# Optimization experiments

Measured on AMD Instinct MI355X. Metric: run time of the kernel, lower is better.

## Reference

```python
import jax, jax.numpy as jnp
import numpy as np

BATCH, IN_SIZE, CH, DIM, MODES, LAYERS, PROJ, OUT = 16, 1, 128, 128, 32, 4, 128, 1


def setup_inputs() -> dict:
    key = jax.random.key(0)
    ks = jax.random.split(key, 12)
    scale = 1.0 / (CH * CH)
    inp = {
        "z": jax.random.normal(ks[0], (BATCH, IN_SIZE, DIM, DIM), dtype=jnp.float32),
        # Lifting: pointwise linear input_size -> channels
        "lift_w": jax.random.normal(ks[1], (CH, IN_SIZE), dtype=jnp.float32) / np.sqrt(IN_SIZE),
        "lift_b": jnp.zeros((CH,), dtype=jnp.float32),
        # Spectral conv weights per layer, two mode corners, complex stored as real/imag
        "wr1": scale * jax.random.normal(ks[2], (LAYERS, CH, CH, MODES, MODES), dtype=jnp.float32),
        "wi1": scale * jax.random.normal(ks[3], (LAYERS, CH, CH, MODES, MODES), dtype=jnp.float32),
        "wr2": scale * jax.random.normal(ks[4], (LAYERS, CH, CH, MODES, MODES), dtype=jnp.float32),
        "wi2": scale * jax.random.normal(ks[5], (LAYERS, CH, CH, MODES, MODES), dtype=jnp.float32),
        # Projection: channels -> projection_size -> output_size (pointwise MLP)
        "pw1": jax.random.normal(ks[6], (PROJ, CH), dtype=jnp.float32) / np.sqrt(CH),
        "pb1": jnp.zeros((PROJ,), dtype=jnp.float32),
        "pw2": jax.random.normal(ks[7], (OUT, PROJ), dtype=jnp.float32) / np.sqrt(PROJ),
        "pb2": jnp.zeros((OUT,), dtype=jnp.float32),
    }
    return inp


def _spectral_conv(v, w1, w2, modes, size):
    # v: [b, c, X, Y] real; rfft2 over last two dims (norm='backward')
    vf = jnp.fft.rfft2(v, norm="backward")  # [b, c, X, Y//2+1] complex
    of = jnp.zeros_like(vf)
    # low-frequency corner
    of = of.at[:, :, :modes, :modes].set(
        jnp.einsum("bixy,ioxy->boxy", vf[:, :, :modes, :modes], w1))
    # high (negative) frequency corner along first spatial axis
    of = of.at[:, :, -modes:, :modes].set(
        jnp.einsum("bixy,ioxy->boxy", vf[:, :, -modes:, :modes], w2))
    return jnp.fft.irfft2(of, s=(size, size), norm="backward")


def reference(z, lift_w, lift_b, wr1, wi1, wr2, wi2, pw1, pb1, pw2, pb2):
    n_layers = wr1.shape[0]
    modes = wr1.shape[-1]
    size = z.shape[-1]
    # Lifting: [b, in, x, y] -> [b, ch, x, y]
    v = jnp.einsum("bixy,ci->bcxy", z, lift_w) + lift_b[None, :, None, None]
    out = v
    for l in range(n_layers):
        w1 = wr1[l] + 1j * wi1[l]
        w2 = wr2[l] + 1j * wi2[l]
        out = _spectral_conv(out, w1, w2, modes, size)
    # Projection MLP (pointwise over grid)
    h = jnp.einsum("bcxy,pc->bpxy", out, pw1) + pb1[None, :, None, None]
    h = jax.nn.gelu(h)
    out = jnp.einsum("bpxy,op->boxy", h, pw2) + pb2[None, :, None, None]
    return out
```

## Files before the change

kernel.cpp:

```cpp
#include <hip/hip_runtime.h>
#include <math.h>

#define B 16
#define CH 128
#define DIM 128
#define MODES 32
#define NLAYERS 4
#define PROJ 128
#define U 64
#define KY 32
#define NMODE (U*KY)
#define N2 (DIM*DIM)
#define PG 32
#define PPG (PROJ/PG)

__device__ __forceinline__ void async16(const void* g, void* l) {
  __builtin_amdgcn_global_load_lds((const __attribute__((address_space(1))) unsigned int*)g,
                                   (__attribute__((address_space(3))) unsigned int*)l, 16, 0, 0);
}

__global__ __launch_bounds__(256) void k_zf1(const float* __restrict__ z,
                                             float2* __restrict__ t1) {
  __shared__ float zrow[16][DIM];
  __shared__ float2 tw[DIM];
  int bid = blockIdx.x;
  int b = bid >> 3, xt = bid & 7;
  int x0 = xt * 16;
  int t = threadIdx.x;
  if (t < 128) {
    float ang = (float)(2.0 * M_PI) * (float)t / 128.0f;
    tw[t] = make_float2(cosf(ang), sinf(ang));
  }
  for (int e = t; e < 16 * DIM / 4; e += 256)
    ((float4*)&zrow[0][0])[e] = ((const float4*)&z[b * N2 + x0 * DIM])[e];
  __syncthreads();
  #pragma unroll
  for (int j = 0; j < 2; ++j) {
    int it = t + j * 256;
    int x_l = it >> 5, ky = it & 31;
    float tr = 0.f, ti = 0.f;
    for (int y = 0; y < DIM; ++y) {
      float v = zrow[x_l][y];
      float2 w = tw[(ky * y) & 127];
      tr += v * w.x;
      ti -= v * w.y;
    }
    t1[((size_t)b * DIM + x0 + x_l) * KY + ky] = make_float2(tr, ti);
  }
}

__global__ __launch_bounds__(256) void k_zf2(const float2* __restrict__ t1,
                                             float* __restrict__ zfr, float* __restrict__ zfi) {
  __shared__ float2 t1s[DIM][KY];
  __shared__ float2 tw[DIM];
  int bid = blockIdx.x;
  int b = bid >> 1, uh = bid & 1;
  int t = threadIdx.x;
  if (t < 128) {
    float ang = (float)(2.0 * M_PI) * (float)t / 128.0f;
    tw[t] = make_float2(cosf(ang), sinf(ang));
  }
  for (int e = t; e < DIM * KY / 2; e += 256)
    ((float4*)&t1s[0][0])[e] = ((const float4*)&t1[(size_t)b * DIM * KY])[e];
  __syncthreads();
  #pragma unroll
  for (int j = 0; j < 4; ++j) {
    int m = t + j * 256;
    int u_l = m >> 5, ky = m & 31;
    int u = uh * 32 + u_l;
    int kx = (u < 32) ? u : (u + 64);
    float ar = 0.f, ai = 0.f;
    for (int x = 0; x < DIM; ++x) {
      float2 v = t1s[x][ky];
      float2 w = tw[(kx * x) & 127];
      ar += v.x * w.x + v.y * w.y;
      ai += v.y * w.x - v.x * w.y;
    }
    zfr[b * NMODE + u * KY + ky] = ar;
    zfi[b * NMODE + u * KY + ky] = ai;
  }
}

__global__ __launch_bounds__(256) void k_lift(const float* __restrict__ zfr, const float* __restrict__ zfi,
                                              const float* __restrict__ lw, const float* __restrict__ lb,
                                              float2* __restrict__ vcout) {
  int idx = blockIdx.x * 256 + threadIdx.x;
  if (idx >= B * CH * NMODE) return;
  int m = idx & (NMODE - 1);
  int c = (idx >> 11) & 127;
  int b = idx >> 18;
  float w = lw[c];
  float re = w * zfr[b * NMODE + m];
  float im = w * zfi[b * NMODE + m];
  if (m == 0) re += 16384.f * lb[c];
  vcout[idx] = make_float2(re, im);
}

__global__ __launch_bounds__(256) void k_spec(const float2* __restrict__ vc,
                                              const float* __restrict__ wr1, const float* __restrict__ wi1,
                                              const float* __restrict__ wr2, const float* __restrict__ wi2,
                                              float2* __restrict__ oc) {
  __shared__ float lW[2][2][2][8][32];
  __shared__ float2 lV[2][2][16][32];
  int bid = blockIdx.x;
  int u = ((bid & 7) << 3) | ((bid >> 3) & 7);
  int ot = bid >> 6;
  int o0 = ot * 8;
  int kxw = u & 31;
  const float* wr = (u >= 32) ? wr2 : wr1;
  const float* wi = (u >= 32) ? wi2 : wi1;
  int t = threadIdx.x;
  int ky = t & 31, bh = (t >> 5) & 1, oq = t >> 6;
  int wv = t >> 6, lane = t & 63;
  float accR[2][8] = {}, accI[2][8] = {};

  #define STAGE(bf, i0)                                                              \
    {                                                                                \
      _Pragma("unroll")                                                              \
      for (int n = 0; n < 3; ++n) {                                                  \
        int nu = wv * 3 + n;                                                         \
        if (nu < 4) {                                                                \
          int ri = nu >> 1, il = nu & 1;                                             \
          int o_l = lane >> 3, ky4 = (lane & 7) * 4;                                 \
          const float* src = (ri ? wi : wr) +                                        \
            (((size_t)((i0) + il) * CH + o0 + o_l) * MODES + kxw) * MODES + ky4;     \
          async16(src, (char*)&lW[bf][0][0][0][0] + (size_t)nu * 1024 + lane * 16);  \
        } else {                                                                     \
          int nv = nu - 4;                                                           \
          int il = nv >> 2;                                                          \
          int b_l = (nv & 3) * 4 + (lane >> 4), ky2 = (lane & 15) * 2;               \
          const float2* src = vc + ((size_t)b_l * CH + (i0) + il) * NMODE +          \
                              u * KY + ky2;                                          \
          async16(src, (char*)&lV[bf][0][0][0] + (size_t)nv * 1024 + lane * 16);     \
        }                                                                            \
      }                                                                              \
    }

  STAGE(0, 0);
  for (int k = 0; k < 64; ++k) {
    int cur = k & 1;
    __syncthreads();
    if (k + 1 < 64) STAGE(cur ^ 1, (k + 1) * 2);
    #pragma unroll
    for (int il = 0; il < 2; ++il) {
      float wrv[2], wiv[2];
      #pragma unroll
      for (int j = 0; j < 2; ++j) {
        wrv[j] = lW[cur][0][il][oq * 2 + j][ky];
        wiv[j] = lW[cur][1][il][oq * 2 + j][ky];
      }
      #pragma unroll
      for (int bb = 0; bb < 8; ++bb) {
        float2 v = lV[cur][il][bh * 8 + bb][ky];
        #pragma unroll
        for (int j = 0; j < 2; ++j) {
          accR[j][bb] += wrv[j] * v.x - wiv[j] * v.y;
          accI[j][bb] += wrv[j] * v.y + wiv[j] * v.x;
        }
      }
    }
  }
  #undef STAGE
  #pragma unroll
  for (int j = 0; j < 2; ++j)
    #pragma unroll
    for (int bb = 0; bb < 8; ++bb) {
      int o = o0 + oq * 2 + j, b = bh * 8 + bb;
      oc[(((size_t)b * CH + o) * U + u) * KY + ky] = make_float2(accR[j][bb], accI[j][bb]);
    }
}

__global__ __launch_bounds__(256) void k_proj0(float2* __restrict__ vc) {
  int idx = blockIdx.x * 256 + threadIdx.x;
  if (idx >= B * CH * 33) return;
  int pi = idx % 33;
  int bc = idx / 33;
  float2* base = vc + (size_t)bc * NMODE;
  if (pi == 0) {
    base[0].y = 0.f;
  } else if (pi == 32) {
    base[32 * KY].x *= 0.5f;
    base[32 * KY].y *= 0.5f;
  } else {
    int ua = pi, ub = 64 - pi;
    float2 a = base[ua * KY], b2 = base[ub * KY];
    base[ua * KY] = make_float2(0.5f * (a.x + b2.x), 0.5f * (a.y - b2.y));
    base[ub * KY] = make_float2(0.5f * (b2.x + a.x), 0.5f * (b2.y - a.y));
  }
}

__global__ __launch_bounds__(256) void k_pw1(const float2* __restrict__ xc,
                                             const float* __restrict__ pw1,
                                             float2* __restrict__ hc) {
  __shared__ float wT[CH][CH + 1];
  int bid = blockIdx.x;
  int b = ((bid & 7) << 1) | ((bid >> 8) & 1);
  int jt = (bid >> 3) & 31;
  int t = threadIdx.x;
  for (int e = t; e < CH * CH; e += 256) {
    int p = e >> 7, c = e & 127;
    wT[c][p] = pw1[e];
  }
  __syncthreads();
  int tx = t & 15, ty = t >> 4;
  int j0 = jt * 64 + tx * 4;
  float accR[4][8] = {}, accI[4][8] = {};
  for (int c = 0; c < CH; ++c) {
    const float4* x4 = (const float4*)&xc[((size_t)b * CH + c) * NMODE + j0];
    float4 v0 = x4[0], v1 = x4[1];
    float xrv[4] = {v0.x, v0.z, v1.x, v1.z};
    float xiv[4] = {v0.y, v0.w, v1.y, v1.w};
    float w[8];
    #pragma unroll
    for (int pp = 0; pp < 8; ++pp) w[pp] = wT[c][ty * 8 + pp];
    #pragma unroll
    for (int jj = 0; jj < 4; ++jj)
      #pragma unroll
      for (int pp = 0; pp < 8; ++pp) {
        accR[jj][pp] += w[pp] * xrv[jj];
        accI[jj][pp] += w[pp] * xiv[jj];
      }
  }
  #pragma unroll
  for (int pp = 0; pp < 8; ++pp) {
    int p = ty * 8 + pp;
    float4* o4 = (float4*)&hc[((size_t)b * CH + p) * NMODE + j0];
    o4[0] = make_float4(accR[0][pp], accI[0][pp], accR[1][pp], accI[1][pp]);
    o4[1] = make_float4(accR[2][pp], accI[2][pp], accR[3][pp], accI[3][pp]);
  }
}

__global__ __launch_bounds__(256) void k_idft_partial(const float2* __restrict__ hc,
                                                      const float* __restrict__ pb1,
                                                      const float* __restrict__ pw2,
                                                      float* __restrict__ partial) {
  __shared__ float2 tw[DIM];
  __shared__ float2 hfs[2][NMODE];
  __shared__ float2 sbuf[16][KY];
  int bid = blockIdx.x;
  int b = (bid & 7) | (((bid >> 3) & 1) << 3);
  int pg = (bid >> 4) & 31, xs = bid >> 9;
  int x0 = xs * 8;
  int t = threadIdx.x;
  int wv = t >> 6, lane = t & 63;
  if (t < 128) {
    float ang = (float)(2.0 * M_PI) * (float)t / 128.0f;
    tw[t] = make_float2(cosf(ang), sinf(ang));
  }

  #define STAGE_H(bf, pp_)                                                           \
    {                                                                                \
      const char* srcb = (const char*)(hc + ((size_t)b * CH + pg * PPG + (pp_)) * NMODE); \
      _Pragma("unroll")                                                              \
      for (int n = 0; n < 4; ++n) {                                                  \
        int nu = wv * 4 + n;                                                         \
        async16(srcb + (size_t)nu * 1024 + lane * 16,                                \
                (char*)&hfs[bf][0] + (size_t)nu * 1024 + lane * 16);                 \
      }                                                                              \
    }

  STAGE_H(0, 0);
  __syncthreads();
  int y = t & 63, xh = t >> 6;
  float Cr[KY], Sr[KY];
  #pragma unroll
  for (int ky = 0; ky < KY; ++ky) {
    float2 w = tw[(ky * y) & 127];
    float wk = (ky == 0) ? 1.f : 2.f;
    Cr[ky] = wk * w.x;
    Sr[ky] = -wk * w.y;
  }
  int xqA = t >> 5, kyA = t & 31;
  int xA = x0 + xqA;
  float res[8] = {0.f, 0.f, 0.f, 0.f, 0.f, 0.f, 0.f, 0.f};
  for (int pp = 0; pp < PPG; ++pp) {
    int p = pg * PPG + pp;
    int cur = pp & 1;
    if (pp) __syncthreads();
    if (pp + 1 < PPG) STAGE_H(cur ^ 1, pp + 1);
    {
      float per = 0.f, pei = 0.f, por = 0.f, poi = 0.f;
      #pragma unroll
      for (int uu = 0; uu < 32; uu += 2) {
        float2 w0 = tw[(uu * xA) & 127];
        float2 h0 = hfs[cur][uu * KY + kyA];
        per += h0.x * w0.x - h0.y * w0.y;
        pei += h0.x * w0.y + h0.y * w0.x;
        float2 w1 = tw[((uu + 1) * xA) & 127];
        float2 h1 = hfs[cur][(uu + 1) * KY + kyA];
        por += h1.x * w1.x - h1.y * w1.y;
        poi += h1.x * w1.y + h1.y * w1.x;
      }
      #pragma unroll
      for (int uu = 32; uu < 64; uu += 2) {
        float2 w0 = tw[((uu + 64) * xA) & 127];
        float2 h0 = hfs[cur][uu * KY + kyA];
        per += h0.x * w0.x - h0.y * w0.y;
        pei += h0.x * w0.y + h0.y * w0.x;
        float2 w1 = tw[((uu + 65) * xA) & 127];
        float2 h1 = hfs[cur][(uu + 1) * KY + kyA];
        por += h1.x * w1.x - h1.y * w1.y;
        poi += h1.x * w1.y + h1.y * w1.x;
      }
      sbuf[xqA][kyA]     = make_float2(per + por, pei + poi);
      sbuf[xqA + 8][kyA] = make_float2(per - por, pei - poi);
    }
    __syncthreads();
    float pb = pb1[p], pw = pw2[p];
    #pragma unroll
    for (int sl = 0; sl < 4; ++sl) {
      int s_i = xh + sl * 4;
      float ae = 0.f, ao = 0.f;
      #pragma unroll
      for (int ky = 0; ky < KY; ky += 2) {
        float4 v = *(const float4*)&sbuf[s_i][ky];
        ae += v.x * Cr[ky] + v.y * Sr[ky];
        ao += v.z * Cr[ky + 1] + v.w * Sr[ky + 1];
      }
      float hlo = (ae + ao) * (1.f / 16384.f) + pb;
      float hhi = (ae - ao) * (1.f / 16384.f) + pb;
      float zlo = 1.5957691216057308f * (hlo + 0.044715f * hlo * hlo * hlo);
      float zhi = 1.5957691216057308f * (hhi + 0.044715f * hhi * hhi * hhi);
      res[sl * 2]     += pw * hlo * __builtin_amdgcn_rcpf(1.f + __expf(-zlo));
      res[sl * 2 + 1] += pw * hhi * __builtin_amdgcn_rcpf(1.f + __expf(-zhi));
    }
  }
  #undef STAGE_H
  size_t pbase = ((size_t)pg * B + b) * N2;
  #pragma unroll
  for (int sl = 0; sl < 4; ++sl) {
    int s_i = xh + sl * 4;
    int x = x0 + (s_i & 7) + ((s_i >> 3) << 6);
    partial[pbase + x * DIM + y]      = res[sl * 2];
    partial[pbase + x * DIM + y + 64] = res[sl * 2 + 1];
  }
}

__global__ __launch_bounds__(256) void k_reduce(const float* __restrict__ partial,
                                                const float* __restrict__ pb2,
                                                float* __restrict__ outp) {
  int idx = blockIdx.x * 256 + threadIdx.x;
  if (idx >= B * N2) return;
  float s = pb2[0];
  #pragma unroll
  for (int pg = 0; pg < PG; ++pg) s += partial[(size_t)pg * B * N2 + idx];
  outp[idx] = s;
}

extern "C" void kernel_launch(void* const* d_in, const int* in_sizes, int n_in,
                              void* d_out, int out_size, void* d_ws, size_t ws_size,
                              hipStream_t stream) {
  const float* z   = (const float*)d_in[0];
  const float* lw  = (const float*)d_in[1];
  const float* lb  = (const float*)d_in[2];
  const float* wr1 = (const float*)d_in[3];
  const float* wi1 = (const float*)d_in[4];
  const float* wr2 = (const float*)d_in[5];
  const float* wi2 = (const float*)d_in[6];
  const float* pw1 = (const float*)d_in[7];
  const float* pb1 = (const float*)d_in[8];
  const float* pw2 = (const float*)d_in[9];
  const float* pb2 = (const float*)d_in[10];
  float* out = (float*)d_out;
  float* ws = (float*)d_ws;

  float* zfr = ws;
  float* zfi = zfr + 32768;
  float2* Ac = (float2*)(ws + 65536);
  float2* Bc = Ac + (size_t)B * CH * NMODE;
  float2* t1 = Bc;

  k_zf1<<<B * 8, 256, 0, stream>>>(z, t1);
  k_zf2<<<B * 2, 256, 0, stream>>>(t1, zfr, zfi);
  k_lift<<<(B * CH * NMODE) / 256, 256, 0, stream>>>(zfr, zfi, lw, lb, Ac);

  const size_t WSTRIDE = (size_t)CH * CH * MODES * MODES;
  float2 *ir = Ac, *oc = Bc;
  for (int l = 0; l < NLAYERS; ++l) {
    k_spec<<<1024, 256, 0, stream>>>(ir,
                                     wr1 + l * WSTRIDE, wi1 + l * WSTRIDE,
                                     wr2 + l * WSTRIDE, wi2 + l * WSTRIDE,
                                     oc);
    if (l < NLAYERS - 1)
      k_proj0<<<(B * CH * 33 + 255) / 256, 256, 0, stream>>>(oc);
    float2* tmp = ir; ir = oc; oc = tmp;
  }
  k_pw1<<<512, 256, 0, stream>>>(ir, pw1, oc);
  float* partial = (float*)ir;
  k_idft_partial<<<B * PG * 8, 256, 0, stream>>>(oc, pb1, pw2, partial);
  k_reduce<<<(B * N2) / 256, 256, 0, stream>>>(partial, pb2, out);
}
```

Baseline: 827.8 us.

## Retile spectral mode-mixing kernel with 4-deep async LDS ring buffer

The spectral mode-mixing kernel now gives each block 8 kx modes, 4 output channels and 4 batches, instead of 1 mode, 8 output channels and all 16 batches. It walks the 128 input channels one at a time through a 4-slot LDS ring filled by async global-to-LDS loads. Three stages stay in flight, gated by explicit vmcnt waits, with one barrier per step. The aim is to hide memory latency and make the weight loads contiguous (1 KB runs per output channel). The cost is that each weight slice is now fetched by four batch-quarter blocks instead of one, which raises weight traffic unless it hits in cache.

```diff
diff --git a/kernel.cpp b/kernel.cpp
--- a/kernel.cpp
+++ b/kernel.cpp
@@ -100,73 +100,78 @@
                                               const float* __restrict__ wr1, const float* __restrict__ wi1,
                                               const float* __restrict__ wr2, const float* __restrict__ wi2,
                                               float2* __restrict__ oc) {
-  __shared__ float lW[2][2][2][8][32];
-  __shared__ float2 lV[2][2][16][32];
-  int bid = blockIdx.x;
-  int u = ((bid & 7) << 3) | ((bid >> 3) & 7);
-  int ot = bid >> 6;
-  int o0 = ot * 8;
-  int kxw = u & 31;
-  const float* wr = (u >= 32) ? wr2 : wr1;
-  const float* wi = (u >= 32) ? wi2 : wi1;
-  int t = threadIdx.x;
-  int ky = t & 31, bh = (t >> 5) & 1, oq = t >> 6;
+  __shared__ float4 ring[4][1024];
+  int bid = blockIdx.x;
+  int g = bid & 7;
+  int r = bid >> 3;
+  int ot = r & 31, bq = r >> 5;
+  int o0 = ot * 4, b0 = bq * 4;
+  int u0 = g * 8;
+  int kxw0 = (g & 3) * 8;
+  const float* wr = (g >= 4) ? wr2 : wr1;
+  const float* wi = (g >= 4) ? wi2 : wi1;
+  int t = threadIdx.x;
+  int u_l = t >> 5, ky = t & 31;
   int wv = t >> 6, lane = t & 63;
-  float accR[2][8] = {}, accI[2][8] = {};
-
-  #define STAGE(bf, i0)                                                              \
-    {                                                                                \
+  float accR[4][4] = {}, accI[4][4] = {};
+
+  #define STAGE(c)                                                                   \
+    if ((c) < 128) {                                                                 \
+      char* dst0 = (char*)&ring[(c) & 3][0];                                         \
       _Pragma("unroll")                                                              \
-      for (int n = 0; n < 3; ++n) {                                                  \
-        int nu = wv * 3 + n;                                                         \
-        if (nu < 4) {                                                                \
-          int ri = nu >> 1, il = nu & 1;                                             \
-          int o_l = lane >> 3, ky4 = (lane & 7) * 4;                                 \
+      for (int n = 0; n < 4; ++n) {                                                  \
+        int nu = wv * 4 + n;                                                         \
+        if (nu < 8) {                                                                \
+          int o_l = nu >> 1, ri = nu & 1;                                            \
           const float* src = (ri ? wi : wr) +                                        \
-            (((size_t)((i0) + il) * CH + o0 + o_l) * MODES + kxw) * MODES + ky4;     \
-          async16(src, (char*)&lW[bf][0][0][0][0] + (size_t)nu * 1024 + lane * 16);  \
+            (((size_t)(c) * CH + o0 + o_l) * MODES + kxw0) * MODES;                  \
+          async16(src + lane * 4, dst0 + nu * 1024 + lane * 16);                     \
         } else {                                                                     \
-          int nv = nu - 4;                                                           \
-          int il = nv >> 2;                                                          \
-          int b_l = (nv & 3) * 4 + (lane >> 4), ky2 = (lane & 15) * 2;               \
-          const float2* src = vc + ((size_t)b_l * CH + (i0) + il) * NMODE +          \
-                              u * KY + ky2;                                          \
-          async16(src, (char*)&lV[bf][0][0][0] + (size_t)nv * 1024 + lane * 16);     \
+          int nv = nu - 8;                                                           \
+          int b_l = nv >> 1, hf = nv & 1;                                            \
+          const float2* src = vc + ((size_t)(b0 + b_l) * CH + (c)) * NMODE +         \
+                              (u0 + hf * 4) * KY;                                    \
+          async16(src + lane * 2, dst0 + 8192 + nv * 1024 + lane * 16);              \
         }                                                                            \
       }                                                                              \
     }
 
-  STAGE(0, 0);
-  for (int k = 0; k < 64; ++k) {
-    int cur = k & 1;
-    __syncthreads();
-    if (k + 1 < 64) STAGE(cur ^ 1, (k + 1) * 2);
+  STAGE(0); STAGE(1); STAGE(2);
+  for (int k = 0; k < 128; ++k) {
+    __builtin_amdgcn_sched_barrier(0);
+    if (k < 126)       asm volatile("s_waitcnt vmcnt(8)" ::: "memory");
+    else if (k == 126) asm volatile("s_waitcnt vmcnt(4)" ::: "memory");
+    else               asm volatile("s_waitcnt vmcnt(0)" ::: "memory");
+    __builtin_amdgcn_s_barrier();
+    __builtin_amdgcn_sched_barrier(0);
+    STAGE(k + 3);
+    {
+      const float*  Wb = (const float*)&ring[k & 3][0];
+      const float2* Vb = (const float2*)((const char*)&ring[k & 3][0] + 8192);
+      float2 vv[4];
+      #pragma unroll
+      for (int bb = 0; bb < 4; ++bb)
+        vv[bb] = Vb[(bb * 2 + (u_l >> 2)) * 128 + (u_l & 3) * 32 + ky];
+      #pragma unroll
+      for (int oo = 0; oo < 4; ++oo) {
+        float wrv = Wb[(oo * 2 + 0) * 256 + t];
+        float wiv = Wb[(oo * 2 + 1) * 256 + t];
+        #pragma unroll
+        for (int bb = 0; bb < 4; ++bb) {
+          accR[oo][bb] += wrv * vv[bb].x - wiv * vv[bb].y;
+          accI[oo][bb] += wrv * vv[bb].y + wiv * vv[bb].x;
+        }
+      }
+    }
+  }
+  #undef STAGE
+  int u = u0 + u_l;
+  #pragma unroll
+  for (int oo = 0; oo < 4; ++oo)
     #pragma unroll
-    for (int il = 0; il < 2; ++il) {
-      float wrv[2], wiv[2];
-      #pragma unroll
-      for (int j = 0; j < 2; ++j) {
-        wrv[j] = lW[cur][0][il][oq * 2 + j][ky];
-        wiv[j] = lW[cur][1][il][oq * 2 + j][ky];
-      }
-      #pragma unroll
-      for (int bb = 0; bb < 8; ++bb) {
-        float2 v = lV[cur][il][bh * 8 + bb][ky];
-        #pragma unroll
-        for (int j = 0; j < 2; ++j) {
-          accR[j][bb] += wrv[j] * v.x - wiv[j] * v.y;
-          accI[j][bb] += wrv[j] * v.y + wiv[j] * v.x;
-        }
-      }
-    }
-  }
-  #undef STAGE
-  #pragma unroll
-  for (int j = 0; j < 2; ++j)
-    #pragma unroll
-    for (int bb = 0; bb < 8; ++bb) {
-      int o = o0 + oq * 2 + j, b = bh * 8 + bb;
-      oc[(((size_t)b * CH + o) * U + u) * KY + ky] = make_float2(accR[j][bb], accI[j][bb]);
+    for (int bb = 0; bb < 4; ++bb) {
+      int o = o0 + oo, b = b0 + bb;
+      oc[(((size_t)b * CH + o) * U + u) * KY + ky] = make_float2(accR[oo][bb], accI[oo][bb]);
     }
 }
 
```

Result: slower. 1.340 ms (+61.9%).

## Deepen spectral weight pipeline to 4-stage ring; precompute iDFT twiddles

Applied to the files above, without the earlier changes.

The spectral mixing kernel replaces its double buffer with a four-slot LDS ring that keeps three stages of async global-to-LDS loads in flight. It syncs with explicit vmcnt waits and raw s_barrier instead of __syncthreads. This is meant to hide global load latency better. The inverse DFT kernel precomputes the per-row twiddle factors for the kx sum into a small shared table of float4 pairs, replacing per-iteration indexed twiddle lookups and address arithmetic. Risks include larger LDS use lowering occupancy and the correctness of the hand-counted vmcnt values.

```diff
diff --git a/kernel.cpp b/kernel.cpp
--- a/kernel.cpp
+++ b/kernel.cpp
@@ -100,8 +100,7 @@
                                               const float* __restrict__ wr1, const float* __restrict__ wi1,
                                               const float* __restrict__ wr2, const float* __restrict__ wi2,
                                               float2* __restrict__ oc) {
-  __shared__ float lW[2][2][2][8][32];
-  __shared__ float2 lV[2][2][16][32];
+  __shared__ float4 ring[4][768];
   int bid = blockIdx.x;
   int u = ((bid & 7) << 3) | ((bid >> 3) & 7);
   int ot = bid >> 6;
@@ -114,8 +113,10 @@
   int wv = t >> 6, lane = t & 63;
   float accR[2][8] = {}, accI[2][8] = {};
 
-  #define STAGE(bf, i0)                                                              \
-    {                                                                                \
+  #define STAGE(c)                                                                   \
+    if ((c) < 64) {                                                                  \
+      char* dst0 = (char*)&ring[0][0] + (size_t)((c) & 3) * 12288;                   \
+      int i0_ = (c) * 2;                                                             \
       _Pragma("unroll")                                                              \
       for (int n = 0; n < 3; ++n) {                                                  \
         int nu = wv * 3 + n;                                                         \
@@ -123,39 +124,49 @@
           int ri = nu >> 1, il = nu & 1;                                             \
           int o_l = lane >> 3, ky4 = (lane & 7) * 4;                                 \
           const float* src = (ri ? wi : wr) +                                        \
-            (((size_t)((i0) + il) * CH + o0 + o_l) * MODES + kxw) * MODES + ky4;     \
-          async16(src, (char*)&lW[bf][0][0][0][0] + (size_t)nu * 1024 + lane * 16);  \
+            (((size_t)(i0_ + il) * CH + o0 + o_l) * MODES + kxw) * MODES + ky4;      \
+          async16(src, dst0 + nu * 1024 + lane * 16);                                \
         } else {                                                                     \
           int nv = nu - 4;                                                           \
           int il = nv >> 2;                                                          \
           int b_l = (nv & 3) * 4 + (lane >> 4), ky2 = (lane & 15) * 2;               \
-          const float2* src = vc + ((size_t)b_l * CH + (i0) + il) * NMODE +          \
+          const float2* src = vc + ((size_t)b_l * CH + i0_ + il) * NMODE +           \
                               u * KY + ky2;                                          \
-          async16(src, (char*)&lV[bf][0][0][0] + (size_t)nv * 1024 + lane * 16);     \
+          async16(src, dst0 + 4096 + nv * 1024 + lane * 16);                         \
         }                                                                            \
       }                                                                              \
     }
 
-  STAGE(0, 0);
+  STAGE(0); STAGE(1); STAGE(2);
   for (int k = 0; k < 64; ++k) {
-    int cur = k & 1;
-    __syncthreads();
-    if (k + 1 < 64) STAGE(cur ^ 1, (k + 1) * 2);
-    #pragma unroll
-    for (int il = 0; il < 2; ++il) {
-      float wrv[2], wiv[2];
+    __builtin_amdgcn_sched_barrier(0);
+    if (k < 62)       asm volatile("s_waitcnt vmcnt(6)" ::: "memory");
+    else if (k == 62) asm volatile("s_waitcnt vmcnt(3)" ::: "memory");
+    else              asm volatile("s_waitcnt vmcnt(0)" ::: "memory");
+    __builtin_amdgcn_s_barrier();
+    __builtin_amdgcn_sched_barrier(0);
+    STAGE(k + 3);
+    {
+      const char* dstc = (const char*)&ring[0][0] + (size_t)(k & 3) * 12288;
+      const float*  Wb = (const float*)dstc;
+      const float2* Vb = (const float2*)(dstc + 4096);
       #pragma unroll
-      for (int j = 0; j < 2; ++j) {
-        wrv[j] = lW[cur][0][il][oq * 2 + j][ky];
-        wiv[j] = lW[cur][1][il][oq * 2 + j][ky];
-      }
-      #pragma unroll
-      for (int bb = 0; bb < 8; ++bb) {
-        float2 v = lV[cur][il][bh * 8 + bb][ky];
+      for (int il = 0; il < 2; ++il) {
+        float wrv[2], wiv[2];
         #pragma unroll
         for (int j = 0; j < 2; ++j) {
-          accR[j][bb] += wrv[j] * v.x - wiv[j] * v.y;
-          accI[j][bb] += wrv[j] * v.y + wiv[j] * v.x;
+          wrv[j] = Wb[il * 256 + (oq * 2 + j) * 32 + ky];
+          wiv[j] = Wb[(2 + il) * 256 + (oq * 2 + j) * 32 + ky];
+        }
+        #pragma unroll
+        for (int bb = 0; bb < 8; ++bb) {
+          int b = bh * 8 + bb;
+          float2 v = Vb[il * 512 + (b >> 2) * 128 + (b & 3) * 32 + ky];
+          #pragma unroll
+          for (int j = 0; j < 2; ++j) {
+            accR[j][bb] += wrv[j] * v.x - wiv[j] * v.y;
+            accI[j][bb] += wrv[j] * v.y + wiv[j] * v.x;
+          }
         }
       }
     }
@@ -237,6 +248,7 @@
   __shared__ float2 tw[DIM];
   __shared__ float2 hfs[2][NMODE];
   __shared__ float2 sbuf[16][KY];
+  __shared__ float4 sE[8][32];
   int bid = blockIdx.x;
   int b = (bid & 7) | (((bid >> 3) & 1) << 3);
   int pg = (bid >> 4) & 31, xs = bid >> 9;
@@ -261,6 +273,14 @@
 
   STAGE_H(0, 0);
   __syncthreads();
+  {
+    int xq = t >> 5, j = t & 31;
+    int x = x0 + xq;
+    int kxE = (j < 16) ? (2 * j) : (2 * j + 64);
+    float2 wE = tw[(kxE * x) & 127];
+    float2 wO = tw[((kxE + 1) * x) & 127];
+    sE[xq][j] = make_float4(wE.x, wE.y, wO.x, wO.y);
+  }
   int y = t & 63, xh = t >> 6;
   float Cr[KY], Sr[KY];
   #pragma unroll
@@ -270,8 +290,8 @@
     Cr[ky] = wk * w.x;
     Sr[ky] = -wk * w.y;
   }
+  __syncthreads();
   int xqA = t >> 5, kyA = t & 31;
-  int xA = x0 + xqA;
   float res[8] = {0.f, 0.f, 0.f, 0.f, 0.f, 0.f, 0.f, 0.f};
   for (int pp = 0; pp < PPG; ++pp) {
     int p = pg * PPG + pp;
@@ -281,26 +301,14 @@
     {
       float per = 0.f, pei = 0.f, por = 0.f, poi = 0.f;
       #pragma unroll
-      for (int uu = 0; uu < 32; uu += 2) {
-        float2 w0 = tw[(uu * xA) & 127];
-        float2 h0 = hfs[cur][uu * KY + kyA];
-        per += h0.x * w0.x - h0.y * w0.y;
-        pei += h0.x * w0.y + h0.y * w0.x;
-        float2 w1 = tw[((uu + 1) * xA) & 127];
-        float2 h1 = hfs[cur][(uu + 1) * KY + kyA];
-        por += h1.x * w1.x - h1.y * w1.y;
-        poi += h1.x * w1.y + h1.y * w1.x;
-      }
-      #pragma unroll
-      for (int uu = 32; uu < 64; uu += 2) {
-        float2 w0 = tw[((uu + 64) * xA) & 127];
-        float2 h0 = hfs[cur][uu * KY + kyA];
-        per += h0.x * w0.x - h0.y * w0.y;
-        pei += h0.x * w0.y + h0.y * w0.x;
-        float2 w1 = tw[((uu + 65) * xA) & 127];
-        float2 h1 = hfs[cur][(uu + 1) * KY + kyA];
-        por += h1.x * w1.x - h1.y * w1.y;
-        poi += h1.x * w1.y + h1.y * w1.x;
+      for (int j = 0; j < 32; ++j) {
+        float4 E = sE[xqA][j];
+        float2 h0 = hfs[cur][(2 * j) * KY + kyA];
+        float2 h1 = hfs[cur][(2 * j + 1) * KY + kyA];
+        per += h0.x * E.x - h0.y * E.y;
+        pei += h0.x * E.y + h0.y * E.x;
+        por += h1.x * E.z - h1.y * E.w;
+        poi += h1.x * E.w + h1.y * E.z;
       }
       sbuf[xqA][kyA]     = make_float2(per + por, pei + poi);
       sbuf[xqA + 8][kyA] = make_float2(per - por, pei - poi);
```

Result: slower. 915.3 us (+10.6%).
